# Optimization experiments

Hardware: AMD Instinct MI355X
Metric: run time of the kernel (lower is better)

## Reference

```python
import jax, jax.numpy as jnp
import numpy as np

N = 50000      # total nodes (actors) across batch
E = 300000     # edges surviving the distance threshold
N_AGT = 128    # n_actor
N_CTX = 128    # n_ctx == n_actor for A2A
EPS = 1e-5


def _gn(x, gamma, beta):
    # torch GroupNorm(num_groups=1) on a [N, C] tensor: normalize over C per row
    mu = jnp.mean(x, axis=-1, keepdims=True)
    var = jnp.mean((x - mu) ** 2, axis=-1, keepdims=True)
    return (x - mu) * jax.lax.rsqrt(var + EPS) * gamma + beta


def setup_inputs() -> dict:
    key = jax.random.key(0)
    ks = jax.random.split(key, 16)
    s = 0.02
    f32 = jnp.float32
    inp = {
        'agts': jax.random.normal(ks[0], (N, N_AGT), f32),
        'ctx': jax.random.normal(ks[1], (N, N_CTX), f32),
        'agt_ctrs': jax.random.normal(ks[2], (N, 2), f32),
        'ctx_ctrs': jax.random.normal(ks[3], (N, 2), f32),
        'hi': jax.random.randint(ks[4], (E,), 0, N, dtype=jnp.int32),
        'wi': jax.random.randint(ks[5], (E,), 0, N, dtype=jnp.int32),
        # dist: nn.Linear(2, n_ctx) -> ReLU -> Linear(n_ctx, n_ctx, GN, act)
        'w_d1': jax.random.normal(ks[6], (N_CTX, 2), f32) * s,
        'b_d1': jnp.zeros((N_CTX,), f32),
        'w_d2': jax.random.normal(ks[7], (N_CTX, N_CTX), f32) * s,
        'g_d2': jnp.ones((N_CTX,), f32), 'bt_d2': jnp.zeros((N_CTX,), f32),
        # query: Linear(n_agt, n_ctx, GN, act)
        'w_q': jax.random.normal(ks[8], (N_CTX, N_AGT), f32) * s,
        'g_q': jnp.ones((N_CTX,), f32), 'bt_q': jnp.zeros((N_CTX,), f32),
        # ctx: Linear(3*n_ctx, n_agt, GN, act) -> nn.Linear(n_agt, n_agt, bias=False)
        'w_c1': jax.random.normal(ks[9], (N_AGT, 3 * N_CTX), f32) * s,
        'g_c1': jnp.ones((N_AGT,), f32), 'bt_c1': jnp.zeros((N_AGT,), f32),
        'w_c2': jax.random.normal(ks[10], (N_AGT, N_AGT), f32) * s,
        # agt: nn.Linear(n_agt, n_agt, bias=False)
        'w_a': jax.random.normal(ks[11], (N_AGT, N_AGT), f32) * s,
        # norm: GroupNorm(1, n_agt)
        'g_n': jnp.ones((N_AGT,), f32), 'bt_n': jnp.zeros((N_AGT,), f32),
        # linear: Linear(n_agt, n_agt, GN, act=False)
        'w_l': jax.random.normal(ks[12], (N_AGT, N_AGT), f32) * s,
        'g_l': jnp.ones((N_AGT,), f32), 'bt_l': jnp.zeros((N_AGT,), f32),
    }
    return inp


def reference(agts, ctx, agt_ctrs, ctx_ctrs, hi, wi,
              w_d1, b_d1, w_d2, g_d2, bt_d2,
              w_q, g_q, bt_q,
              w_c1, g_c1, bt_c1, w_c2,
              w_a, g_n, bt_n,
              w_l, g_l, bt_l):
    res = agts
    # edge-wise distance features: [E, 2] -> [E, n_ctx]
    d = agt_ctrs[hi] - ctx_ctrs[wi]
    d = jax.nn.relu(d @ w_d1.T + b_d1)
    d = jax.nn.relu(_gn(d @ w_d2.T, g_d2, bt_d2))
    # edge-wise query from gathered target nodes: [E, n_ctx]
    q = jax.nn.relu(_gn(agts[hi] @ w_q.T, g_q, bt_q))
    # fuse dist/query/context: [E, 3*n_ctx] -> [E, n_agt]
    e = jnp.concatenate([d, q, ctx[wi]], axis=-1)
    e = jax.nn.relu(_gn(e @ w_c1.T, g_c1, bt_c1))
    e = e @ w_c2.T
    # scatter-add messages back to nodes
    out = agts @ w_a.T
    out = out.at[hi].add(e)
    out = jax.nn.relu(_gn(out, g_n, bt_n))
    out = _gn(out @ w_l.T, g_l, bt_l)
    return jax.nn.relu(out + res)
```

## Files before the change

### kernel.cpp

```cpp
#include <hip/hip_runtime.h>
#include <hip/hip_bf16.h>

#define NCH 128
#define EB  32
#define NB  32

typedef __attribute__((ext_vector_type(8))) short bf16x8;
typedef __attribute__((ext_vector_type(4))) float f32x4;

__device__ inline unsigned short f2bf(float v) {
    __hip_bfloat16 h = __float2bfloat16(v);
    return __builtin_bit_cast(unsigned short, h);
}

__device__ inline bf16x8 cvt8(const float* __restrict__ p) {
    bf16x8 r;
#pragma unroll
    for (int i = 0; i < 8; ++i) r[i] = (short)f2bf(p[i]);
    return r;
}

template<bool BF>
__device__ inline bf16x8 load_row8(const void* __restrict__ src, int node, int koff) {
    if constexpr (BF)
        return *(const bf16x8*)((const unsigned short*)src + (size_t)node * NCH + koff);
    else
        return cvt8((const float*)src + (size_t)node * NCH + koff);
}

__global__ __launch_bounds__(256) void convert_weights_kernel(
    const float* __restrict__ w_d2, const float* __restrict__ w_q,
    const float* __restrict__ w_c1, const float* __restrict__ w_c2,
    const float* __restrict__ w_a,  const float* __restrict__ w_l,
    unsigned short* __restrict__ out)
{
    int i = blockIdx.x * 256 + threadIdx.x;
    const float* src; int off;
    if      (i < 16384)  { src = w_d2; off = i; }
    else if (i < 32768)  { src = w_q;  off = i - 16384; }
    else if (i < 81920)  { src = w_c1; off = i - 32768; }
    else if (i < 98304)  { src = w_c2; off = i - 81920; }
    else if (i < 114688) { src = w_a;  off = i - 98304; }
    else if (i < 131072) { src = w_l;  off = i - 114688; }
    else return;
    out[i] = f2bf(src[off]);
}

__global__ __launch_bounds__(256) void convert_ctx_kernel(
    const float* __restrict__ c, unsigned short* __restrict__ cbf, int nq)
{
    const int stride = gridDim.x * blockDim.x;
    for (int i = blockIdx.x * blockDim.x + threadIdx.x; i < nq; i += stride) {
        float4 v = ((const float4*)c)[i];
        ushort4 o = { f2bf(v.x), f2bf(v.y), f2bf(v.z), f2bf(v.w) };
        ((ushort4*)cbf)[i] = o;
    }
}

__device__ inline void gemm_k128_lds(const unsigned short* __restrict__ A,
                                     const unsigned short* __restrict__ W,
                                     int lane, int wave, f32x4 (&acc)[2][2])
{
#pragma unroll
    for (int k = 0; k < 4; ++k) {
        const int koff = k * 32 + (lane >> 4) * 8;
        bf16x8 a[2], b[2];
#pragma unroll
        for (int m = 0; m < 2; ++m) {
            int r = m * 16 + (lane & 15);
            int byte = (r * 256 + koff * 2) ^ ((r & 7) << 4);
            a[m] = *(const bf16x8*)((const char*)A + byte);
        }
#pragma unroll
        for (int n = 0; n < 2; ++n) {
            int wr = wave * 32 + n * 16 + (lane & 15);
            b[n] = *(const bf16x8*)(W + (size_t)wr * NCH + koff);
        }
#pragma unroll
        for (int m = 0; m < 2; ++m)
#pragma unroll
            for (int n = 0; n < 2; ++n)
                acc[m][n] = __builtin_amdgcn_mfma_f32_16x16x32_bf16(a[m], b[n], acc[m][n], 0, 0, 0);
    }
}

__device__ inline void gn_frag_stats(const f32x4 (&acc)[2][2],
                                     float (*red_s)[4], float (*red_q)[4],
                                     int t, float (&mu)[2][4], float (&rs)[2][4])
{
    const int lane = t & 63, wave = t >> 6;
    float s[2][4], q[2][4];
#pragma unroll
    for (int m = 0; m < 2; ++m)
#pragma unroll
        for (int j = 0; j < 4; ++j) {
            float sv = acc[m][0][j] + acc[m][1][j];
            float qv = acc[m][0][j] * acc[m][0][j] + acc[m][1][j] * acc[m][1][j];
#pragma unroll
            for (int off = 1; off < 16; off <<= 1) {
                sv += __shfl_xor(sv, off);
                qv += __shfl_xor(qv, off);
            }
            s[m][j] = sv; q[m][j] = qv;
        }
    if ((lane & 15) == 0) {
        const int rg = lane >> 4;
#pragma unroll
        for (int m = 0; m < 2; ++m)
#pragma unroll
            for (int j = 0; j < 4; ++j) {
                int r = m * 16 + rg * 4 + j;
                red_s[r][wave] = s[m][j];
                red_q[r][wave] = q[m][j];
            }
    }
    __syncthreads();
#pragma unroll
    for (int m = 0; m < 2; ++m)
#pragma unroll
        for (int j = 0; j < 4; ++j) {
            int r = m * 16 + ((lane >> 4) << 2) + j;
            float4 sv = *(const float4*)red_s[r];
            float4 qv = *(const float4*)red_q[r];
            float ssum = (sv.x + sv.y) + (sv.z + sv.w);
            float qsum = (qv.x + qv.y) + (qv.z + qv.w);
            float m_  = ssum * (1.f / NCH);
            float var = qsum * (1.f / NCH) - m_ * m_;
            mu[m][j] = m_;
            rs[m][j] = rsqrtf(var + 1e-5f);
        }
}

__device__ inline void gn_pack_store(const f32x4 (&acc)[2][2],
                                     const float (&mu)[2][4], const float (&rs)[2][4],
                                     const float* __restrict__ gamma,
                                     const float* __restrict__ beta,
                                     unsigned short* __restrict__ dst, int t)
{
    const int lane = t & 63, wave = t >> 6;
    const int c0 = wave * 32 + (lane & 15);
    const float g0 = gamma[c0],      b0 = beta[c0];
    const float g1 = gamma[c0 + 16], b1 = beta[c0 + 16];
#pragma unroll
    for (int m = 0; m < 2; ++m)
#pragma unroll
        for (int j = 0; j < 4; ++j) {
            int r = m * 16 + ((lane >> 4) << 2) + j;
            float v0 = fmaxf((acc[m][0][j] - mu[m][j]) * rs[m][j] * g0 + b0, 0.f);
            float v1 = fmaxf((acc[m][1][j] - mu[m][j]) * rs[m][j] * g1 + b1, 0.f);
            unsigned int p0 = f2bf(v0), p1 = f2bf(v1);
            unsigned int o0 = (unsigned int)__shfl_xor((int)p0, 1);
            unsigned int o1 = (unsigned int)__shfl_xor((int)p1, 1);
            if (!(lane & 1)) {
                int cb = c0 * 2;
                int byte0 = (r * 256 + cb) ^ ((r & 7) << 4);
                int byte1 = (r * 256 + cb + 32) ^ ((r & 7) << 4);
                *(unsigned int*)((char*)dst + byte0) = (p0 & 0xffffu) | (o0 << 16);
                *(unsigned int*)((char*)dst + byte1) = (p1 & 0xffffu) | (o1 << 16);
            }
        }
    __syncthreads();
}

__global__ __launch_bounds__(256) void node_prep_kernel(
    const float* __restrict__ agts,
    const unsigned short* __restrict__ wa_bf, const unsigned short* __restrict__ wq_bf,
    const float* __restrict__ g_q, const float* __restrict__ bt_q,
    float* __restrict__ outbuf, unsigned short* __restrict__ qbf, int N)
{
    const int t = threadIdx.x;
    const int lane = t & 63, wave = t >> 6;
    const int n0 = blockIdx.x * NB;

    __shared__ __align__(16) float red_s[NB][4];
    __shared__ __align__(16) float red_q[NB][4];

    int r0 = n0 + (lane & 15);      if (r0 >= N) r0 = N - 1;
    int r1 = n0 + 16 + (lane & 15); if (r1 >= N) r1 = N - 1;

    const f32x4 z = { 0.f, 0.f, 0.f, 0.f };
    f32x4 accO[2][2] = { { z, z }, { z, z } };
    f32x4 accQ[2][2] = { { z, z }, { z, z } };
#pragma unroll
    for (int k = 0; k < 4; ++k) {
        const int koff = k * 32 + (lane >> 4) * 8;
        bf16x8 a[2], bo[2], bq[2];
        a[0] = load_row8<false>(agts, r0, koff);
        a[1] = load_row8<false>(agts, r1, koff);
#pragma unroll
        for (int n = 0; n < 2; ++n) {
            int wr = wave * 32 + n * 16 + (lane & 15);
            bo[n] = *(const bf16x8*)(wa_bf + (size_t)wr * NCH + koff);
            bq[n] = *(const bf16x8*)(wq_bf + (size_t)wr * NCH + koff);
        }
#pragma unroll
        for (int m = 0; m < 2; ++m)
#pragma unroll
            for (int n = 0; n < 2; ++n) {
                accO[m][n] = __builtin_amdgcn_mfma_f32_16x16x32_bf16(a[m], bo[n], accO[m][n], 0, 0, 0);
                accQ[m][n] = __builtin_amdgcn_mfma_f32_16x16x32_bf16(a[m], bq[n], accQ[m][n], 0, 0, 0);
            }
    }
#pragma unroll
    for (int m = 0; m < 2; ++m)
#pragma unroll
        for (int n = 0; n < 2; ++n)
#pragma unroll
            for (int j = 0; j < 4; ++j) {
                int r = m * 16 + ((lane >> 4) << 2) + j;
                int ng = n0 + r;
                if (ng < N)
                    outbuf[(size_t)ng * NCH + wave * 32 + n * 16 + (lane & 15)] = accO[m][n][j];
            }
    float mu[2][4], rs[2][4];
    gn_frag_stats(accQ, red_s, red_q, t, mu, rs);
    const int c0 = wave * 32 + (lane & 15);
    const float g0 = g_q[c0],      b0 = bt_q[c0];
    const float g1 = g_q[c0 + 16], b1 = bt_q[c0 + 16];
#pragma unroll
    for (int m = 0; m < 2; ++m)
#pragma unroll
        for (int j = 0; j < 4; ++j) {
            int r = m * 16 + ((lane >> 4) << 2) + j;
            int ng = n0 + r;
            float v0 = fmaxf((accQ[m][0][j] - mu[m][j]) * rs[m][j] * g0 + b0, 0.f);
            float v1 = fmaxf((accQ[m][1][j] - mu[m][j]) * rs[m][j] * g1 + b1, 0.f);
            unsigned int p0 = f2bf(v0), p1 = f2bf(v1);
            unsigned int o0 = (unsigned int)__shfl_xor((int)p0, 1);
            unsigned int o1 = (unsigned int)__shfl_xor((int)p1, 1);
            if (!(lane & 1) && ng < N) {
                unsigned int* rowp = (unsigned int*)((char*)qbf + (size_t)ng * 256);
                rowp[c0 >> 1]        = (p0 & 0xffffu) | (o0 << 16);
                rowp[(c0 + 16) >> 1] = (p1 & 0xffffu) | (o1 << 16);
            }
        }
}

template<bool BIG>
__global__ __launch_bounds__(256, 8) void edge_kernel(
    const void* __restrict__ qsrc, const void* __restrict__ ctx_nb,
    const float* __restrict__ agt_ctrs, const float* __restrict__ ctx_ctrs,
    const int* __restrict__ hi, const int* __restrict__ wi,
    const float* __restrict__ w_d1, const float* __restrict__ b_d1,
    const float* __restrict__ g_d2, const float* __restrict__ bt_d2,
    const float* __restrict__ g_q, const float* __restrict__ bt_q,
    const float* __restrict__ g_c1, const float* __restrict__ bt_c1,
    const unsigned short* __restrict__ wbf,
    float* __restrict__ outbuf, int E)
{
    const int t = threadIdx.x;
    const int lane = t & 63;
    const int wave = t >> 6;
    const int e0 = blockIdx.x * EB;

    __shared__ unsigned short bfQ[EB * NCH];
    __shared__ unsigned short bfD[EB * NCH];
    __shared__ unsigned short bfX[EB * NCH];
    __shared__ __align__(16) float red_s[EB][4];
    __shared__ __align__(16) float red_q[EB][4];
    __shared__ int   sh_h[EB], sh_w[EB];
    __shared__ float sh_dx[EB], sh_dy[EB];

    const unsigned short* Wd2 = wbf;
    const unsigned short* Wq  = wbf + 16384;
    const unsigned short* Wc1 = wbf + 32768;
    const unsigned short* Wc2 = wbf + 81920;

    if (t < EB) {
        int e = e0 + t; if (e >= E) e = E - 1;
        int h = hi[e], w = wi[e];
        sh_h[t] = h; sh_w[t] = w;
        sh_dx[t] = agt_ctrs[2 * h]     - ctx_ctrs[2 * w];
        sh_dy[t] = agt_ctrs[2 * h + 1] - ctx_ctrs[2 * w + 1];
    }
    __syncthreads();

    {
        const int r  = t >> 3;
        const int cc = t & 7;
        const int h = sh_h[r], w = sh_w[r];
#pragma unroll
        for (int half = 0; half < 2; ++half) {
            int c = cc + half * 8;
            bf16x8 qv = load_row8<BIG>(qsrc, h, c * 8);
            bf16x8 xv = load_row8<BIG>(ctx_nb, w, c * 8);
            int byte = (r * 256 + c * 16) ^ ((r & 7) << 4);
            *(bf16x8*)((char*)bfQ + byte) = qv;
            *(bf16x8*)((char*)bfX + byte) = xv;
        }
    }
    {
        const int c = t & 127, rh = t >> 7;
        const float wa = w_d1[2 * c], wb = w_d1[2 * c + 1], bb = b_d1[c];
#pragma unroll
        for (int i = 0; i < 16; ++i) {
            int r = rh * 16 + i;
            float v = fmaxf(fmaf(wa, sh_dx[r], fmaf(wb, sh_dy[r], bb)), 0.f);
            unsigned int pv = f2bf(v);
            unsigned int ov = (unsigned int)__shfl_xor((int)pv, 1);
            if (!(c & 1)) {
                int byte = (r * 256 + c * 2) ^ ((r & 7) << 4);
                *(unsigned int*)((char*)bfD + byte) = (pv & 0xffffu) | (ov << 16);
            }
        }
    }
    __syncthreads();

    const f32x4 z = { 0.f, 0.f, 0.f, 0.f };
    f32x4 acc[2][2];
    float mu[2][4], rs[2][4];

    acc[0][0] = z; acc[0][1] = z; acc[1][0] = z; acc[1][1] = z;
    gemm_k128_lds(bfD, Wd2, lane, wave, acc);
    gn_frag_stats(acc, red_s, red_q, t, mu, rs);
    gn_pack_store(acc, mu, rs, g_d2, bt_d2, bfD, t);

    if constexpr (!BIG) {
        acc[0][0] = z; acc[0][1] = z; acc[1][0] = z; acc[1][1] = z;
        gemm_k128_lds(bfQ, Wq, lane, wave, acc);
        gn_frag_stats(acc, red_s, red_q, t, mu, rs);
        gn_pack_store(acc, mu, rs, g_q, bt_q, bfQ, t);
    }

    acc[0][0] = z; acc[0][1] = z; acc[1][0] = z; acc[1][1] = z;
#pragma unroll
    for (int kt = 0; kt < 12; ++kt) {
        const unsigned short* Ab = (kt < 4) ? bfD : (kt < 8) ? bfQ : bfX;
        const int koff = (kt & 3) * 32 + (lane >> 4) * 8;
        bf16x8 a[2], b[2];
#pragma unroll
        for (int m = 0; m < 2; ++m) {
            int r = m * 16 + (lane & 15);
            int byte = (r * 256 + koff * 2) ^ ((r & 7) << 4);
            a[m] = *(const bf16x8*)((const char*)Ab + byte);
        }
#pragma unroll
        for (int n = 0; n < 2; ++n) {
            int wr = wave * 32 + n * 16 + (lane & 15);
            b[n] = *(const bf16x8*)(Wc1 + (size_t)wr * 384 + kt * 32 + (lane >> 4) * 8);
        }
#pragma unroll
        for (int m = 0; m < 2; ++m)
#pragma unroll
            for (int n = 0; n < 2; ++n)
                acc[m][n] = __builtin_amdgcn_mfma_f32_16x16x32_bf16(a[m], b[n], acc[m][n], 0, 0, 0);
    }
    gn_frag_stats(acc, red_s, red_q, t, mu, rs);
    gn_pack_store(acc, mu, rs, g_c1, bt_c1, bfD, t);

    acc[0][0] = z; acc[0][1] = z; acc[1][0] = z; acc[1][1] = z;
    gemm_k128_lds(bfD, Wc2, lane, wave, acc);
#pragma unroll
    for (int m = 0; m < 2; ++m)
#pragma unroll
        for (int n = 0; n < 2; ++n)
#pragma unroll
            for (int j = 0; j < 4; ++j) {
                int r = m * 16 + ((lane >> 4) << 2) + j;
                if (e0 + r < E)
                    atomicAdd(&outbuf[(size_t)sh_h[r] * NCH + wave * 32 + n * 16 + (lane & 15)],
                              acc[m][n][j]);
            }
}

__global__ __launch_bounds__(256) void node_init_kernel(
    const float* __restrict__ agts, const unsigned short* __restrict__ wa_bf,
    float* __restrict__ outbuf, int N)
{
    const int t = threadIdx.x;
    const int lane = t & 63, wave = t >> 6;
    const int n0 = blockIdx.x * NB;

    int r0 = n0 + (lane & 15);      if (r0 >= N) r0 = N - 1;
    int r1 = n0 + 16 + (lane & 15); if (r1 >= N) r1 = N - 1;

    const f32x4 z = { 0.f, 0.f, 0.f, 0.f };
    f32x4 acc[2][2] = { { z, z }, { z, z } };
#pragma unroll
    for (int k = 0; k < 4; ++k) {
        const int koff = k * 32 + (lane >> 4) * 8;
        bf16x8 a[2], b[2];
        a[0] = load_row8<false>(agts, r0, koff);
        a[1] = load_row8<false>(agts, r1, koff);
#pragma unroll
        for (int n = 0; n < 2; ++n) {
            int wr = wave * 32 + n * 16 + (lane & 15);
            b[n] = *(const bf16x8*)(wa_bf + (size_t)wr * NCH + koff);
        }
#pragma unroll
        for (int m = 0; m < 2; ++m)
#pragma unroll
            for (int n = 0; n < 2; ++n)
                acc[m][n] = __builtin_amdgcn_mfma_f32_16x16x32_bf16(a[m], b[n], acc[m][n], 0, 0, 0);
    }
#pragma unroll
    for (int m = 0; m < 2; ++m)
#pragma unroll
        for (int n = 0; n < 2; ++n)
#pragma unroll
            for (int j = 0; j < 4; ++j) {
                int r = m * 16 + ((lane >> 4) << 2) + j;
                int ng = n0 + r;
                if (ng < N)
                    outbuf[(size_t)ng * NCH + wave * 32 + n * 16 + (lane & 15)] = acc[m][n][j];
            }
}

__global__ __launch_bounds__(256) void node_post_kernel(
    float* __restrict__ outbuf, const float* __restrict__ agts,
    const float* __restrict__ g_n, const float* __restrict__ bt_n,
    const unsigned short* __restrict__ wl_bf,
    const float* __restrict__ g_l, const float* __restrict__ bt_l, int N)
{
    const int t = threadIdx.x;
    const int lane = t & 63, wave = t >> 6;
    const int n0 = blockIdx.x * NB;

    __shared__ unsigned short bfP[NB * NCH];
    __shared__ __align__(16) float red_s[NB][4];
    __shared__ __align__(16) float red_q[NB][4];

    const int c = t & 127, rh = t >> 7;
    float v[16];
#pragma unroll
    for (int i = 0; i < 16; ++i) {
        int n = n0 + rh * 16 + i; if (n >= N) n = N - 1;
        v[i] = outbuf[(size_t)n * NCH + c];
    }
#pragma unroll
    for (int i = 0; i < 16; ++i) {
        float s = v[i], q = v[i] * v[i];
        for (int off = 32; off > 0; off >>= 1) {
            s += __shfl_down(s, off);
            q += __shfl_down(q, off);
        }
        if (lane == 0) { red_s[rh * 16 + i][wave & 1] = s; red_q[rh * 16 + i][wave & 1] = q; }
    }
    __syncthreads();
    {
        const float g = g_n[c], b = bt_n[c];
#pragma unroll
        for (int i = 0; i < 16; ++i) {
            int r = rh * 16 + i;
            float s = red_s[r][0] + red_s[r][1];
            float q = red_q[r][0] + red_q[r][1];
            float m_  = s * (1.f / NCH);
            float var = q * (1.f / NCH) - m_ * m_;
            float rrs = rsqrtf(var + 1e-5f);
            float val = fmaxf((v[i] - m_) * rrs * g + b, 0.f);
            unsigned int pv = f2bf(val);
            unsigned int ov = (unsigned int)__shfl_xor((int)pv, 1);
            if (!(c & 1)) {
                int byte = (r * 256 + c * 2) ^ ((r & 7) << 4);
                *(unsigned int*)((char*)bfP + byte) = (pv & 0xffffu) | (ov << 16);
            }
        }
    }
    __syncthreads();

    const f32x4 z = { 0.f, 0.f, 0.f, 0.f };
    f32x4 acc[2][2] = { { z, z }, { z, z } };
    gemm_k128_lds(bfP, wl_bf, lane, wave, acc);

    float mu[2][4], rs[2][4];
    gn_frag_stats(acc, red_s, red_q, t, mu, rs);
    const int c0 = wave * 32 + (lane & 15);
    const float g0 = g_l[c0],      b0 = bt_l[c0];
    const float g1 = g_l[c0 + 16], b1 = bt_l[c0 + 16];
#pragma unroll
    for (int m = 0; m < 2; ++m)
#pragma unroll
        for (int j = 0; j < 4; ++j) {
            int r = m * 16 + ((lane >> 4) << 2) + j;
            int ng = n0 + r;
            if (ng < N) {
                float v0 = (acc[m][0][j] - mu[m][j]) * rs[m][j] * g0 + b0;
                float v1 = (acc[m][1][j] - mu[m][j]) * rs[m][j] * g1 + b1;
                v0 = fmaxf(v0 + agts[(size_t)ng * NCH + c0], 0.f);
                v1 = fmaxf(v1 + agts[(size_t)ng * NCH + c0 + 16], 0.f);
                outbuf[(size_t)ng * NCH + c0]      = v0;
                outbuf[(size_t)ng * NCH + c0 + 16] = v1;
            }
        }
}

extern "C" void kernel_launch(void* const* d_in, const int* in_sizes, int n_in,
                              void* d_out, int out_size, void* d_ws, size_t ws_size,
                              hipStream_t stream) {
    const float* agts     = (const float*)d_in[0];
    const float* ctx      = (const float*)d_in[1];
    const float* agt_ctrs = (const float*)d_in[2];
    const float* ctx_ctrs = (const float*)d_in[3];
    const int*   hi       = (const int*)d_in[4];
    const int*   wi       = (const int*)d_in[5];
    const float* w_d1     = (const float*)d_in[6];
    const float* b_d1     = (const float*)d_in[7];
    const float* w_d2     = (const float*)d_in[8];
    const float* g_d2     = (const float*)d_in[9];
    const float* bt_d2    = (const float*)d_in[10];
    const float* w_q      = (const float*)d_in[11];
    const float* g_q      = (const float*)d_in[12];
    const float* bt_q     = (const float*)d_in[13];
    const float* w_c1     = (const float*)d_in[14];
    const float* g_c1     = (const float*)d_in[15];
    const float* bt_c1    = (const float*)d_in[16];
    const float* w_c2     = (const float*)d_in[17];
    const float* w_a      = (const float*)d_in[18];
    const float* g_n      = (const float*)d_in[19];
    const float* bt_n     = (const float*)d_in[20];
    const float* w_l      = (const float*)d_in[21];
    const float* g_l      = (const float*)d_in[22];
    const float* bt_l     = (const float*)d_in[23];

    const int N = in_sizes[0] / NCH;
    const int E = in_sizes[4];

    float* outbuf = (float*)d_out;

    unsigned short* wbf = (unsigned short*)d_ws;
    unsigned short* cbf = wbf + 131072;
    unsigned short* qbf = cbf + (size_t)N * NCH;
    const size_t need = 262144ull + (size_t)N * NCH * 4ull;
    const bool big = (d_ws != nullptr) && (ws_size >= need);

    const int nb_nodes = (N + NB - 1) / NB;
    const int nb_edges = (E + EB - 1) / EB;

    convert_weights_kernel<<<512, 256, 0, stream>>>(w_d2, w_q, w_c1, w_c2, w_a, w_l, wbf);

    if (big) {
        convert_ctx_kernel<<<1024, 256, 0, stream>>>(ctx, cbf, N * NCH / 4);
        node_prep_kernel<<<nb_nodes, 256, 0, stream>>>(
            agts, wbf + 98304, wbf + 16384, g_q, bt_q, outbuf, qbf, N);
        edge_kernel<true><<<nb_edges, 256, 0, stream>>>(
            qbf, cbf, agt_ctrs, ctx_ctrs, hi, wi,
            w_d1, b_d1, g_d2, bt_d2, g_q, bt_q, g_c1, bt_c1,
            wbf, outbuf, E);
    } else {
        node_init_kernel<<<nb_nodes, 256, 0, stream>>>(agts, wbf + 98304, outbuf, N);
        edge_kernel<false><<<nb_edges, 256, 0, stream>>>(
            agts, ctx, agt_ctrs, ctx_ctrs, hi, wi,
            w_d1, b_d1, g_d2, bt_d2, g_q, bt_q, g_c1, bt_c1,
            wbf, outbuf, E);
    }
    node_post_kernel<<<nb_nodes, 256, 0, stream>>>(
        outbuf, agts, g_n, bt_n, wbf + 114688, g_l, bt_l, N);
}
```

Before: 324.7 us.

## Precompute per-node Wc1 projections of query and context, gather them in edge kernel

Uses the linearity of the first ctx linear layer to split Wc1 into dist, query and ctx blocks. The query and ctx blocks are applied once per node in node_prep, producing bf16 projections pq and px. The edge kernel then gathers and sums the two 128-wide projections instead of running two K=128 GEMMs per edge, and the separate ctx conversion kernel is removed. Weight conversion reorders w_c1 into three contiguous 128x128 blocks. The cost is an extra per-node GEMM pair and bf16 rounding of the projected values before GroupNorm.

After: 308.9 us. -4.9%, faster.

```diff
diff --git a/kernel.cpp b/kernel.cpp
--- a/kernel.cpp
+++ b/kernel.cpp
@@ -11,6 +11,9 @@
 __device__ inline unsigned short f2bf(float v) {
     __hip_bfloat16 h = __float2bfloat16(v);
     return __builtin_bit_cast(unsigned short, h);
+}
+__device__ inline float bf2f(unsigned short u) {
+    return __builtin_bit_cast(float, (unsigned int)u << 16);
 }
 
 __device__ inline bf16x8 cvt8(const float* __restrict__ p) {
@@ -35,26 +38,17 @@
     unsigned short* __restrict__ out)
 {
     int i = blockIdx.x * 256 + threadIdx.x;
+    if (i >= 131072) return;
     const float* src; int off;
     if      (i < 16384)  { src = w_d2; off = i; }
     else if (i < 32768)  { src = w_q;  off = i - 16384; }
-    else if (i < 81920)  { src = w_c1; off = i - 32768; }
+    else if (i < 49152)  { int j = i - 32768; src = w_c1; off = (j >> 7) * 384 + (j & 127); }
+    else if (i < 65536)  { int j = i - 49152; src = w_c1; off = (j >> 7) * 384 + 128 + (j & 127); }
+    else if (i < 81920)  { int j = i - 65536; src = w_c1; off = (j >> 7) * 384 + 256 + (j & 127); }
     else if (i < 98304)  { src = w_c2; off = i - 81920; }
     else if (i < 114688) { src = w_a;  off = i - 98304; }
-    else if (i < 131072) { src = w_l;  off = i - 114688; }
-    else return;
+    else                 { src = w_l;  off = i - 114688; }
     out[i] = f2bf(src[off]);
-}
-
-__global__ __launch_bounds__(256) void convert_ctx_kernel(
-    const float* __restrict__ c, unsigned short* __restrict__ cbf, int nq)
-{
-    const int stride = gridDim.x * blockDim.x;
-    for (int i = blockIdx.x * blockDim.x + threadIdx.x; i < nq; i += stride) {
-        float4 v = ((const float4*)c)[i];
-        ushort4 o = { f2bf(v.x), f2bf(v.y), f2bf(v.z), f2bf(v.w) };
-        ((ushort4*)cbf)[i] = o;
-    }
 }
 
 __device__ inline void gemm_k128_lds(const unsigned short* __restrict__ A,
@@ -162,18 +156,49 @@
     __syncthreads();
 }
 
+__device__ inline void frag_pack_global(const f32x4 (&acc)[2][2],
+                                        unsigned short* __restrict__ dst,
+                                        int n0, int N, int t)
+{
+    const int lane = t & 63, wave = t >> 6;
+    const int c0 = wave * 32 + (lane & 15);
+#pragma unroll
+    for (int m = 0; m < 2; ++m)
+#pragma unroll
+        for (int j = 0; j < 4; ++j) {
+            int r = m * 16 + ((lane >> 4) << 2) + j;
+            int ng = n0 + r;
+            unsigned int p0 = f2bf(acc[m][0][j]);
+            unsigned int p1 = f2bf(acc[m][1][j]);
+            unsigned int o0 = (unsigned int)__shfl_xor((int)p0, 1);
+            unsigned int o1 = (unsigned int)__shfl_xor((int)p1, 1);
+            if (!(lane & 1) && ng < N) {
+                unsigned int* rowp = (unsigned int*)(dst + (size_t)ng * NCH);
+                rowp[c0 >> 1]        = (p0 & 0xffffu) | (o0 << 16);
+                rowp[(c0 + 16) >> 1] = (p1 & 0xffffu) | (o1 << 16);
+            }
+        }
+}
+
 __global__ __launch_bounds__(256) void node_prep_kernel(
-    const float* __restrict__ agts,
-    const unsigned short* __restrict__ wa_bf, const unsigned short* __restrict__ wq_bf,
+    const float* __restrict__ agts, const float* __restrict__ ctx,
+    const unsigned short* __restrict__ wbf,
     const float* __restrict__ g_q, const float* __restrict__ bt_q,
-    float* __restrict__ outbuf, unsigned short* __restrict__ qbf, int N)
+    float* __restrict__ outbuf,
+    unsigned short* __restrict__ pq, unsigned short* __restrict__ px, int N)
 {
     const int t = threadIdx.x;
     const int lane = t & 63, wave = t >> 6;
     const int n0 = blockIdx.x * NB;
 
+    __shared__ unsigned short bfQ[NB * NCH];
     __shared__ __align__(16) float red_s[NB][4];
     __shared__ __align__(16) float red_q[NB][4];
+
+    const unsigned short* Wq   = wbf + 16384;
+    const unsigned short* Wc1q = wbf + 49152;
+    const unsigned short* Wc1x = wbf + 65536;
+    const unsigned short* Wa   = wbf + 98304;
 
     int r0 = n0 + (lane & 15);      if (r0 >= N) r0 = N - 1;
     int r1 = n0 + 16 + (lane & 15); if (r1 >= N) r1 = N - 1;
@@ -190,8 +215,8 @@
 #pragma unroll
         for (int n = 0; n < 2; ++n) {
             int wr = wave * 32 + n * 16 + (lane & 15);
-            bo[n] = *(const bf16x8*)(wa_bf + (size_t)wr * NCH + koff);
-            bq[n] = *(const bf16x8*)(wq_bf + (size_t)wr * NCH + koff);
+            bo[n] = *(const bf16x8*)(Wa + (size_t)wr * NCH + koff);
+            bq[n] = *(const bf16x8*)(Wq + (size_t)wr * NCH + koff);
         }
 #pragma unroll
         for (int m = 0; m < 2; ++m)
@@ -214,31 +239,148 @@
             }
     float mu[2][4], rs[2][4];
     gn_frag_stats(accQ, red_s, red_q, t, mu, rs);
-    const int c0 = wave * 32 + (lane & 15);
-    const float g0 = g_q[c0],      b0 = bt_q[c0];
-    const float g1 = g_q[c0 + 16], b1 = bt_q[c0 + 16];
-#pragma unroll
-    for (int m = 0; m < 2; ++m)
-#pragma unroll
-        for (int j = 0; j < 4; ++j) {
-            int r = m * 16 + ((lane >> 4) << 2) + j;
-            int ng = n0 + r;
-            float v0 = fmaxf((accQ[m][0][j] - mu[m][j]) * rs[m][j] * g0 + b0, 0.f);
-            float v1 = fmaxf((accQ[m][1][j] - mu[m][j]) * rs[m][j] * g1 + b1, 0.f);
-            unsigned int p0 = f2bf(v0), p1 = f2bf(v1);
-            unsigned int o0 = (unsigned int)__shfl_xor((int)p0, 1);
-            unsigned int o1 = (unsigned int)__shfl_xor((int)p1, 1);
-            if (!(lane & 1) && ng < N) {
-                unsigned int* rowp = (unsigned int*)((char*)qbf + (size_t)ng * 256);
-                rowp[c0 >> 1]        = (p0 & 0xffffu) | (o0 << 16);
-                rowp[(c0 + 16) >> 1] = (p1 & 0xffffu) | (o1 << 16);
-            }
-        }
-}
-
-template<bool BIG>
-__global__ __launch_bounds__(256, 8) void edge_kernel(
-    const void* __restrict__ qsrc, const void* __restrict__ ctx_nb,
+    gn_pack_store(accQ, mu, rs, g_q, bt_q, bfQ, t);
+
+    f32x4 accPq[2][2] = { { z, z }, { z, z } };
+    f32x4 accPx[2][2] = { { z, z }, { z, z } };
+#pragma unroll
+    for (int k = 0; k < 4; ++k) {
+        const int koff = k * 32 + (lane >> 4) * 8;
+        bf16x8 aq[2], ax[2], bq2[2], bx[2];
+#pragma unroll
+        for (int m = 0; m < 2; ++m) {
+            int r = m * 16 + (lane & 15);
+            int byte = (r * 256 + koff * 2) ^ ((r & 7) << 4);
+            aq[m] = *(const bf16x8*)((const char*)bfQ + byte);
+        }
+        ax[0] = load_row8<false>(ctx, r0, koff);
+        ax[1] = load_row8<false>(ctx, r1, koff);
+#pragma unroll
+        for (int n = 0; n < 2; ++n) {
+            int wr = wave * 32 + n * 16 + (lane & 15);
+            bq2[n] = *(const bf16x8*)(Wc1q + (size_t)wr * NCH + koff);
+            bx[n]  = *(const bf16x8*)(Wc1x + (size_t)wr * NCH + koff);
+        }
+#pragma unroll
+        for (int m = 0; m < 2; ++m)
+#pragma unroll
+            for (int n = 0; n < 2; ++n) {
+                accPq[m][n] = __builtin_amdgcn_mfma_f32_16x16x32_bf16(aq[m], bq2[n], accPq[m][n], 0, 0, 0);
+                accPx[m][n] = __builtin_amdgcn_mfma_f32_16x16x32_bf16(ax[m], bx[n], accPx[m][n], 0, 0, 0);
+            }
+    }
+    frag_pack_global(accPq, pq, n0, N, t);
+    frag_pack_global(accPx, px, n0, N, t);
+}
+
+__global__ __launch_bounds__(256) void edge_kernel_pre(
+    const unsigned short* __restrict__ pq, const unsigned short* __restrict__ px,
+    const float* __restrict__ agt_ctrs, const float* __restrict__ ctx_ctrs,
+    const int* __restrict__ hi, const int* __restrict__ wi,
+    const float* __restrict__ w_d1, const float* __restrict__ b_d1,
+    const float* __restrict__ g_d2, const float* __restrict__ bt_d2,
+    const float* __restrict__ g_c1, const float* __restrict__ bt_c1,
+    const unsigned short* __restrict__ wbf,
+    float* __restrict__ outbuf, int E)
+{
+    const int t = threadIdx.x;
+    const int lane = t & 63;
+    const int wave = t >> 6;
+    const int e0 = blockIdx.x * EB;
+
+    __shared__ unsigned short bfD[EB * NCH];
+    __shared__ float S[EB][NCH + 4];
+    __shared__ __align__(16) float red_s[EB][4];
+    __shared__ __align__(16) float red_q[EB][4];
+    __shared__ int   sh_h[EB], sh_w[EB];
+    __shared__ float sh_dx[EB], sh_dy[EB];
+
+    const unsigned short* Wd2  = wbf;
+    const unsigned short* Wc1d = wbf + 32768;
+    const unsigned short* Wc2  = wbf + 81920;
+
+    if (t < EB) {
+        int e = e0 + t; if (e >= E) e = E - 1;
+        int h = hi[e], w = wi[e];
+        sh_h[t] = h; sh_w[t] = w;
+        sh_dx[t] = agt_ctrs[2 * h]     - ctx_ctrs[2 * w];
+        sh_dy[t] = agt_ctrs[2 * h + 1] - ctx_ctrs[2 * w + 1];
+    }
+    __syncthreads();
+
+    {
+        const int r  = t >> 3;
+        const int cc = t & 7;
+        const int h = sh_h[r], w = sh_w[r];
+#pragma unroll
+        for (int half = 0; half < 2; ++half) {
+            int c8 = (cc + half * 8) * 8;
+            bf16x8 aq = load_row8<true>(pq, h, c8);
+            bf16x8 ax = load_row8<true>(px, w, c8);
+#pragma unroll
+            for (int i = 0; i < 8; ++i)
+                S[r][c8 + i] = bf2f((unsigned short)aq[i]) + bf2f((unsigned short)ax[i]);
+        }
+    }
+    {
+        const int c = t & 127, rh = t >> 7;
+        const float wa = w_d1[2 * c], wb = w_d1[2 * c + 1], bb = b_d1[c];
+#pragma unroll
+        for (int i = 0; i < 16; ++i) {
+            int r = rh * 16 + i;
+            float v = fmaxf(fmaf(wa, sh_dx[r], fmaf(wb, sh_dy[r], bb)), 0.f);
+            unsigned int pv = f2bf(v);
+            unsigned int ov = (unsigned int)__shfl_xor((int)pv, 1);
+            if (!(c & 1)) {
+                int byte = (r * 256 + c * 2) ^ ((r & 7) << 4);
+                *(unsigned int*)((char*)bfD + byte) = (pv & 0xffffu) | (ov << 16);
+            }
+        }
+    }
+    __syncthreads();
+
+    const f32x4 z = { 0.f, 0.f, 0.f, 0.f };
+    f32x4 acc[2][2];
+    float mu[2][4], rs[2][4];
+
+    acc[0][0] = z; acc[0][1] = z; acc[1][0] = z; acc[1][1] = z;
+    gemm_k128_lds(bfD, Wd2, lane, wave, acc);
+    gn_frag_stats(acc, red_s, red_q, t, mu, rs);
+    gn_pack_store(acc, mu, rs, g_d2, bt_d2, bfD, t);
+
+    acc[0][0] = z; acc[0][1] = z; acc[1][0] = z; acc[1][1] = z;
+    gemm_k128_lds(bfD, Wc1d, lane, wave, acc);
+    {
+        const int c0 = wave * 32 + (lane & 15);
+#pragma unroll
+        for (int m = 0; m < 2; ++m)
+#pragma unroll
+            for (int j = 0; j < 4; ++j) {
+                int r = m * 16 + ((lane >> 4) << 2) + j;
+                acc[m][0][j] += S[r][c0];
+                acc[m][1][j] += S[r][c0 + 16];
+            }
+    }
+    gn_frag_stats(acc, red_s, red_q, t, mu, rs);
+    gn_pack_store(acc, mu, rs, g_c1, bt_c1, bfD, t);
+
+    acc[0][0] = z; acc[0][1] = z; acc[1][0] = z; acc[1][1] = z;
+    gemm_k128_lds(bfD, Wc2, lane, wave, acc);
+#pragma unroll
+    for (int m = 0; m < 2; ++m)
+#pragma unroll
+        for (int n = 0; n < 2; ++n)
+#pragma unroll
+            for (int j = 0; j < 4; ++j) {
+                int r = m * 16 + ((lane >> 4) << 2) + j;
+                if (e0 + r < E)
+                    atomicAdd(&outbuf[(size_t)sh_h[r] * NCH + wave * 32 + n * 16 + (lane & 15)],
+                              acc[m][n][j]);
+            }
+}
+
+__global__ __launch_bounds__(256) void edge_kernel_fb(
+    const float* __restrict__ agts, const float* __restrict__ ctx,
     const float* __restrict__ agt_ctrs, const float* __restrict__ ctx_ctrs,
     const int* __restrict__ hi, const int* __restrict__ wi,
     const float* __restrict__ w_d1, const float* __restrict__ b_d1,
@@ -263,7 +405,9 @@
 
     const unsigned short* Wd2 = wbf;
     const unsigned short* Wq  = wbf + 16384;
-    const unsigned short* Wc1 = wbf + 32768;
+    const unsigned short* Wc1d = wbf + 32768;
+    const unsigned short* Wc1q = wbf + 49152;
+    const unsigned short* Wc1x = wbf + 65536;
     const unsigned short* Wc2 = wbf + 81920;
 
     if (t < EB) {
@@ -274,7 +418,6 @@
         sh_dy[t] = agt_ctrs[2 * h + 1] - ctx_ctrs[2 * w + 1];
     }
     __syncthreads();
-
     {
         const int r  = t >> 3;
         const int cc = t & 7;
@@ -282,8 +425,8 @@
 #pragma unroll
         for (int half = 0; half < 2; ++half) {
             int c = cc + half * 8;
-            bf16x8 qv = load_row8<BIG>(qsrc, h, c * 8);
-            bf16x8 xv = load_row8<BIG>(ctx_nb, w, c * 8);
+            bf16x8 qv = load_row8<false>(agts, h, c * 8);
+            bf16x8 xv = load_row8<false>(ctx, w, c * 8);
             int byte = (r * 256 + c * 16) ^ ((r & 7) << 4);
             *(bf16x8*)((char*)bfQ + byte) = qv;
             *(bf16x8*)((char*)bfX + byte) = xv;
@@ -315,36 +458,15 @@
     gn_frag_stats(acc, red_s, red_q, t, mu, rs);
     gn_pack_store(acc, mu, rs, g_d2, bt_d2, bfD, t);
 
-    if constexpr (!BIG) {
-        acc[0][0] = z; acc[0][1] = z; acc[1][0] = z; acc[1][1] = z;
-        gemm_k128_lds(bfQ, Wq, lane, wave, acc);
-        gn_frag_stats(acc, red_s, red_q, t, mu, rs);
-        gn_pack_store(acc, mu, rs, g_q, bt_q, bfQ, t);
-    }
-
     acc[0][0] = z; acc[0][1] = z; acc[1][0] = z; acc[1][1] = z;
-#pragma unroll
-    for (int kt = 0; kt < 12; ++kt) {
-        const unsigned short* Ab = (kt < 4) ? bfD : (kt < 8) ? bfQ : bfX;
-        const int koff = (kt & 3) * 32 + (lane >> 4) * 8;
-        bf16x8 a[2], b[2];
-#pragma unroll
-        for (int m = 0; m < 2; ++m) {
-            int r = m * 16 + (lane & 15);
-            int byte = (r * 256 + koff * 2) ^ ((r & 7) << 4);
-            a[m] = *(const bf16x8*)((const char*)Ab + byte);
-        }
-#pragma unroll
-        for (int n = 0; n < 2; ++n) {
-            int wr = wave * 32 + n * 16 + (lane & 15);
-            b[n] = *(const bf16x8*)(Wc1 + (size_t)wr * 384 + kt * 32 + (lane >> 4) * 8);
-        }
-#pragma unroll
-        for (int m = 0; m < 2; ++m)
-#pragma unroll
-            for (int n = 0; n < 2; ++n)
-                acc[m][n] = __builtin_amdgcn_mfma_f32_16x16x32_bf16(a[m], b[n], acc[m][n], 0, 0, 0);
-    }
+    gemm_k128_lds(bfQ, Wq, lane, wave, acc);
+    gn_frag_stats(acc, red_s, red_q, t, mu, rs);
+    gn_pack_store(acc, mu, rs, g_q, bt_q, bfQ, t);
+
+    acc[0][0] = z; acc[0][1] = z; acc[1][0] = z; acc[1][1] = z;
+    gemm_k128_lds(bfD, Wc1d, lane, wave, acc);
+    gemm_k128_lds(bfQ, Wc1q, lane, wave, acc);
+    gemm_k128_lds(bfX, Wc1x, lane, wave, acc);
     gn_frag_stats(acc, red_s, red_q, t, mu, rs);
     gn_pack_store(acc, mu, rs, g_c1, bt_c1, bfD, t);
 
@@ -518,8 +640,8 @@
     float* outbuf = (float*)d_out;
 
     unsigned short* wbf = (unsigned short*)d_ws;
-    unsigned short* cbf = wbf + 131072;
-    unsigned short* qbf = cbf + (size_t)N * NCH;
+    unsigned short* pq  = wbf + 131072;
+    unsigned short* px  = pq + (size_t)N * NCH;
     const size_t need = 262144ull + (size_t)N * NCH * 4ull;
     const bool big = (d_ws != nullptr) && (ws_size >= need);
 
@@ -529,16 +651,15 @@
     convert_weights_kernel<<<512, 256, 0, stream>>>(w_d2, w_q, w_c1, w_c2, w_a, w_l, wbf);
 
     if (big) {
-        convert_ctx_kernel<<<1024, 256, 0, stream>>>(ctx, cbf, N * NCH / 4);
         node_prep_kernel<<<nb_nodes, 256, 0, stream>>>(
-            agts, wbf + 98304, wbf + 16384, g_q, bt_q, outbuf, qbf, N);
-        edge_kernel<true><<<nb_edges, 256, 0, stream>>>(
-            qbf, cbf, agt_ctrs, ctx_ctrs, hi, wi,
-            w_d1, b_d1, g_d2, bt_d2, g_q, bt_q, g_c1, bt_c1,
+            agts, ctx, wbf, g_q, bt_q, outbuf, pq, px, N);
+        edge_kernel_pre<<<nb_edges, 256, 0, stream>>>(
+            pq, px, agt_ctrs, ctx_ctrs, hi, wi,
+            w_d1, b_d1, g_d2, bt_d2, g_c1, bt_c1,
             wbf, outbuf, E);
     } else {
         node_init_kernel<<<nb_nodes, 256, 0, stream>>>(agts, wbf + 98304, outbuf, N);
-        edge_kernel<false><<<nb_edges, 256, 0, stream>>>(
+        edge_kernel_fb<<<nb_edges, 256, 0, stream>>>(
             agts, ctx, agt_ctrs, ctx_ctrs, hi, wi,
             w_d1, b_d1, g_d2, bt_d2, g_q, bt_q, g_c1, bt_c1,
             wbf, outbuf, E);
```
